# Performance work log

Measured on AMD Instinct MI355X. Metric: run time of the kernel, lower is better.

## Reference

```python
import jax, jax.numpy as jnp
import numpy as np

M, C, K, D = 2048, 16, 8, 256  # queries, classes, clusters/class, feature_dim
H1, H2 = D, D // 2             # MLP hidden sizes


def setup_inputs() -> dict:
    key = jax.random.key(0)
    ks = jax.random.split(key, 8)
    s1 = 1.0 / np.sqrt(2 * D)
    s2 = 1.0 / np.sqrt(H1)
    s3 = 1.0 / np.sqrt(H2)
    return {
        "query_features": jax.random.normal(ks[0], (M, D), jnp.float32),
        "prototypes": jax.random.normal(ks[1], (C, K, D), jnp.float32),
        "W1": jax.random.normal(ks[2], (2 * D, H1), jnp.float32) * s1,
        "b1": jnp.zeros((H1,), jnp.float32),
        "W2": jax.random.normal(ks[3], (H1, H2), jnp.float32) * s2,
        "b2": jnp.zeros((H2,), jnp.float32),
        "W3": jax.random.normal(ks[4], (H2, 1), jnp.float32) * s3,
        "b3": jnp.zeros((1,), jnp.float32),
    }


def reference(query_features, prototypes, W1, b1, W2, b2, W3, b3):
    # Attention MLP on concat([query, prototype]) for every (query, class, cluster)
    # pair. Split W1 into the query half and prototype half so we never
    # materialize the [M,C,K,2D] concat; broadcast-add instead.
    d = query_features.shape[-1]
    Wq, Wp = W1[:d], W1[d:]
    qh = query_features @ Wq                      # [M, H1]
    ph = jnp.einsum('ckd,dh->ckh', prototypes, Wp)  # [C, K, H1]
    h = jax.nn.relu(qh[:, None, None, :] + ph[None] + b1)   # [M, C, K, H1]
    h = jax.nn.relu(h @ W2 + b2)                              # [M, C, K, H2]
    scores = (h @ W3)[..., 0] + b3[0]                         # [M, C, K]
    attn = jax.nn.softmax(scores, axis=-1)                    # softmax over clusters
    weighted = jnp.einsum('mck,ckd->mcd', attn, prototypes)   # [M, C, D]
    diff = query_features[:, None, :] - weighted              # [M, C, D]
    distances = jnp.sqrt(jnp.sum(diff * diff, axis=-1))       # [M, C]
    return -distances
```

## Files before the change

kernel.cpp:

```cpp
#include <hip/hip_runtime.h>
#include <hip/hip_fp16.h>
#include <cstdint>

typedef __attribute__((ext_vector_type(8))) _Float16 f16x8;
typedef __attribute__((ext_vector_type(4))) float f32x4;
typedef __attribute__((ext_vector_type(16))) float f32x16;

__device__ __forceinline__ f16x8 cvt8(float4 x, float4 y) {
    f16x8 r;
    r[0] = (_Float16)x.x; r[1] = (_Float16)x.y; r[2] = (_Float16)x.z; r[3] = (_Float16)x.w;
    r[4] = (_Float16)y.x; r[5] = (_Float16)y.y; r[6] = (_Float16)y.z; r[7] = (_Float16)y.w;
    return r;
}

__device__ __forceinline__ f16x8 relu8(f16x8 v) {
    f16x8 z = {};
    return __builtin_elementwise_max(v, z);
}

__global__ __launch_bounds__(256)
void xpose(const float* __restrict__ query,
           const float* __restrict__ prot,
           const float* __restrict__ W1,
           const float* __restrict__ W2,
           const float* __restrict__ b2,
           _Float16* __restrict__ w1t,
           f16x8* __restrict__ w2p,
           float* __restrict__ Gm,
           float* __restrict__ q2) {
    int b = blockIdx.x, t = threadIdx.x;
    if (b < 32) {
        __shared__ _Float16 lt[64][73];
        int bi = b >> 2, bj = b & 3;
        int r0 = bi * 64, c0 = bj * 64;
        #pragma unroll
        for (int it = 0; it < 4; ++it) {
            int row = it * 16 + (t >> 4);
            int c4 = (t & 15) * 4;
            float4 v = *(const float4*)(W1 + (r0 + row) * 256 + c0 + c4);
            lt[row][c4]     = (_Float16)v.x;
            lt[row][c4 + 1] = (_Float16)v.y;
            lt[row][c4 + 2] = (_Float16)v.z;
            lt[row][c4 + 3] = (_Float16)v.w;
        }
        __syncthreads();
        int c = t >> 2, kq = t & 3;
        unsigned short o[16];
        #pragma unroll
        for (int i = 0; i < 16; ++i) {
            union { _Float16 f; unsigned short s; } u;
            u.f = lt[kq * 16 + i][c];
            o[i] = u.s;
        }
        _Float16* dst = w1t + (r0 >= 256 ? 65536 : 0) + (c0 + c) * 256 + (r0 & 255) + kq * 16;
        *(uint4*)dst       = *(uint4*)&o[0];
        *(uint4*)(dst + 8) = *(uint4*)&o[8];
    } else if (b < 49) {
        int chunk = (b - 32) * 256 + t;
        int ks = chunk >> 8, h = (chunk >> 7) & 1, c = chunk & 127;
        f16x8 o = {};
        if (ks < 16) {
            #pragma unroll
            for (int j = 0; j < 8; ++j)
                o[j] = (_Float16)W2[(ks * 16 + h * 8 + j) * 128 + c];
        } else if (h == 0) {
            o[0] = (_Float16)b2[c];
        }
        w2p[chunk] = o;
    } else if (b < 81) {
        int pid = (b - 49) * 32 + (t >> 3), l8 = t & 7;
        int c = pid >> 6, k = (pid >> 3) & 7, kp = pid & 7;
        const float4* pa = (const float4*)(prot + (c * 8 + k) * 256 + l8 * 32);
        const float4* pb = (const float4*)(prot + (c * 8 + kp) * 256 + l8 * 32);
        float s = 0.f;
        #pragma unroll
        for (int i = 0; i < 8; ++i) {
            float4 x = pa[i], y = pb[i];
            s += x.x * y.x + x.y * y.y + x.z * y.z + x.w * y.w;
        }
        s += __shfl_xor(s, 1); s += __shfl_xor(s, 2); s += __shfl_xor(s, 4);
        if (l8 == 0) Gm[pid] = s;
    } else {
        int m = (b - 81) * 32 + (t >> 3), l8 = t & 7;
        const float4* qp = (const float4*)(query + m * 256 + l8 * 32);
        float s = 0.f;
        #pragma unroll
        for (int i = 0; i < 8; ++i) {
            float4 x = qp[i];
            s += x.x * x.x + x.y * x.y + x.z * x.z + x.w * x.w;
        }
        s += __shfl_xor(s, 1); s += __shfl_xor(s, 2); s += __shfl_xor(s, 4);
        if (l8 == 0) q2[m] = s;
    }
}

__global__ __launch_bounds__(256, 2)
void prepg(const float* __restrict__ query,
           const float* __restrict__ prot,
           const _Float16* __restrict__ w1t,
           const float* __restrict__ b1,
           _Float16* __restrict__ qh16,
           float* __restrict__ sqp,
           _Float16* __restrict__ phpk) {
    int b = blockIdx.x, t = threadIdx.x;
    int w = t >> 6, l = t & 63, l15 = l & 15, l4 = l >> 4;
    int mode, row0, col0;
    if (b < 128)      { mode = 0; row0 = (b >> 2) * 64;         col0 = (b & 3) * 64; }
    else if (b < 192) { mode = 1; row0 = ((b - 128) >> 1) * 64; col0 = ((b - 128) & 1) * 64; }
    else              { mode = 2; row0 = ((b - 192) >> 2) * 64; col0 = ((b - 192) & 3) * 64; }
    const float* Asrc = (mode == 2) ? prot : query;
    const _Float16* Bsrc = (mode == 2) ? (w1t + 65536) : w1t;

    f32x4 acc[4];
    #pragma unroll
    for (int nt = 0; nt < 4; ++nt) acc[nt] = (f32x4){0.f, 0.f, 0.f, 0.f};

    for (int ks = 0; ks < 8; ++ks) {
        int row = row0 + w * 16 + l15;
        const float* ap = Asrc + row * 256 + ks * 32 + l4 * 8;
        f16x8 af = cvt8(*(const float4*)ap, *(const float4*)(ap + 4));
        f16x8 bf[4];
        #pragma unroll
        for (int nt = 0; nt < 4; ++nt) {
            int col = col0 + nt * 16 + l15;
            if (mode == 1) {
                const float* bp = prot + col * 256 + ks * 32 + l4 * 8;
                bf[nt] = cvt8(*(const float4*)bp, *(const float4*)(bp + 4));
            } else {
                bf[nt] = *(const f16x8*)(Bsrc + col * 256 + ks * 32 + l4 * 8);
            }
        }
        #pragma unroll
        for (int nt = 0; nt < 4; ++nt)
            acc[nt] = __builtin_amdgcn_mfma_f32_16x16x32_f16(af, bf[nt], acc[nt], 0, 0, 0);
    }
    #pragma unroll
    for (int nt = 0; nt < 4; ++nt)
        #pragma unroll
        for (int j = 0; j < 4; ++j) {
            int row = row0 + w * 16 + l4 * 4 + j;
            int col = col0 + nt * 16 + l15;
            float v = acc[nt][j];
            if (mode == 0)      qh16[row * 256 + col] = (_Float16)v;
            else if (mode == 1) sqp[row * 128 + col] = v;
            else                phpk[(((col >> 4) * 2 + ((col >> 3) & 1)) * 128 + row) * 8
                                     + (col & 7)] = (_Float16)(v + b1[col]);
        }
}

__global__ __launch_bounds__(1024, 1)
void fused3(const _Float16* __restrict__ qh16,
            const uint4* __restrict__ phpk,
            const uint4* __restrict__ w2p,
            const float* __restrict__ sqp,
            const float* __restrict__ q2,
            const float* __restrict__ Gm,
            const float* __restrict__ W3,
            float* __restrict__ out) {
    __shared__ uint4 w2l[4352];
    __shared__ uint4 phl[4096];
    __shared__ float w3l[128];
    __shared__ float spart[2][2][4][128];

    int t = threadIdx.x;
    int wid = t >> 6, l = t & 63;
    int rg = wid & 3, cs = wid >> 2;
    int lk = l & 31, h = l >> 5;
    int ck = rg * 32 + lk;

    for (int i = t; i < 4352; i += 1024) w2l[i] = w2p[i];
    for (int i = t; i < 4096; i += 1024) phl[i] = phpk[i];
    if (t < 128) w3l[t] = W3[t];
    __syncthreads();

    const _Float16* w2lh = (const _Float16*)w2l;
    const _Float16* phlh = (const _Float16*)phl;
    int m0 = blockIdx.x * 8;

    for (int mi = 0; mi < 4; ++mi) {
        int mA = m0 + mi * 2;
        const _Float16* qra = qh16 + mA * 256 + h * 8;
        const _Float16* qrb = qra + 256;

        f32x16 accA = {}, accB = {};

        f16x8 qa[2], qb[2];
        qa[0] = *(const f16x8*)(qra);
        qb[0] = *(const f16x8*)(qrb);
        qa[1] = *(const f16x8*)(qra + 16);
        qb[1] = *(const f16x8*)(qrb + 16);

        #pragma unroll
        for (int ks = 0; ks < 16; ++ks) {
            f16x8 ph = *(const f16x8*)(phlh + ((ks * 2 + h) * 128 + ck) * 8);
            f16x8 aA = relu8(qa[ks & 1] + ph);
            f16x8 aB = relu8(qb[ks & 1] + ph);
            if (ks < 14) {
                qa[ks & 1] = *(const f16x8*)(qra + (ks + 2) * 16);
                qb[ks & 1] = *(const f16x8*)(qrb + (ks + 2) * 16);
            }
            f16x8 bfr = *(const f16x8*)(w2lh + ((ks * 2 + h) * 128 + cs * 32 + lk) * 8);
            accA = __builtin_amdgcn_mfma_f32_32x32x16_f16(bfr, aA, accA, 0, 0, 0);
            accB = __builtin_amdgcn_mfma_f32_32x32x16_f16(bfr, aB, accB, 0, 0, 0);
        }
        {
            f16x8 e = {};
            if (h == 0) e[0] = (_Float16)1.0f;
            f16x8 bfr = *(const f16x8*)(w2lh + ((32 + h) * 128 + cs * 32 + lk) * 8);
            accA = __builtin_amdgcn_mfma_f32_32x32x16_f16(bfr, e, accA, 0, 0, 0);
            accB = __builtin_amdgcn_mfma_f32_32x32x16_f16(bfr, e, accB, 0, 0, 0);
        }

        int buf = mi & 1;
        {
            float s0 = 0.f, s1 = 0.f, s2 = 0.f, s3 = 0.f;
            #pragma unroll
            for (int r = 0; r < 16; r += 4) {
                s0 = fmaf(fmaxf(accA[r + 0], 0.f), w3l[cs * 32 + ((r + 0) & 3) + 8 * ((r + 0) >> 2) + 4 * h], s0);
                s1 = fmaf(fmaxf(accA[r + 1], 0.f), w3l[cs * 32 + ((r + 1) & 3) + 8 * ((r + 1) >> 2) + 4 * h], s1);
                s2 = fmaf(fmaxf(accA[r + 2], 0.f), w3l[cs * 32 + ((r + 2) & 3) + 8 * ((r + 2) >> 2) + 4 * h], s2);
                s3 = fmaf(fmaxf(accA[r + 3], 0.f), w3l[cs * 32 + ((r + 3) & 3) + 8 * ((r + 3) >> 2) + 4 * h], s3);
            }
            float s = (s0 + s1) + (s2 + s3);
            s += __shfl_xor(s, 32);
            if (l < 32) spart[buf][0][cs][ck] = s;
        }
        {
            float s0 = 0.f, s1 = 0.f, s2 = 0.f, s3 = 0.f;
            #pragma unroll
            for (int r = 0; r < 16; r += 4) {
                s0 = fmaf(fmaxf(accB[r + 0], 0.f), w3l[cs * 32 + ((r + 0) & 3) + 8 * ((r + 0) >> 2) + 4 * h], s0);
                s1 = fmaf(fmaxf(accB[r + 1], 0.f), w3l[cs * 32 + ((r + 1) & 3) + 8 * ((r + 1) >> 2) + 4 * h], s1);
                s2 = fmaf(fmaxf(accB[r + 2], 0.f), w3l[cs * 32 + ((r + 2) & 3) + 8 * ((r + 2) >> 2) + 4 * h], s2);
                s3 = fmaf(fmaxf(accB[r + 3], 0.f), w3l[cs * 32 + ((r + 3) & 3) + 8 * ((r + 3) >> 2) + 4 * h], s3);
            }
            float s = (s0 + s1) + (s2 + s3);
            s += __shfl_xor(s, 32);
            if (l < 32) spart[buf][1][cs][ck] = s;
        }
        __syncthreads();

        if (t < 256) {
            int msel = t >> 7, ckk = t & 127, kk = t & 7;
            int m = mA + msel;
            int cg = ckk >> 3;
            float s = spart[buf][msel][0][ckk] + spart[buf][msel][1][ckk]
                    + spart[buf][msel][2][ckk] + spart[buf][msel][3][ckk];
            float mx = s;
            mx = fmaxf(mx, __shfl_xor(mx, 1));
            mx = fmaxf(mx, __shfl_xor(mx, 2));
            mx = fmaxf(mx, __shfl_xor(mx, 4));
            float e = __expf(s - mx);
            float den = e;
            den += __shfl_xor(den, 1); den += __shfl_xor(den, 2); den += __shfl_xor(den, 4);
            float a = e / den;
            float p2 = a * sqp[m * 128 + ckk];
            float p3 = 0.f;
            #pragma unroll
            for (int kq = 0; kq < 8; ++kq) {
                float ak = __shfl(a, (l & 56) | kq);
                p3 = fmaf(ak, Gm[cg * 64 + kq * 8 + kk], p3);
            }
            p3 *= a;
            float pr = p3 - 2.f * p2;
            pr += __shfl_xor(pr, 1); pr += __shfl_xor(pr, 2); pr += __shfl_xor(pr, 4);
            if (kk == 0)
                out[m * 16 + cg] = -sqrtf(fmaxf(q2[m] + pr, 0.f));
        }
    }
}

extern "C" void kernel_launch(void* const* d_in, const int* in_sizes, int n_in,
                              void* d_out, int out_size, void* d_ws, size_t ws_size,
                              hipStream_t stream) {
    const float* query = (const float*)d_in[0];
    const float* prot  = (const float*)d_in[1];
    const float* W1    = (const float*)d_in[2];
    const float* b1    = (const float*)d_in[3];
    const float* W2    = (const float*)d_in[4];
    const float* b2    = (const float*)d_in[5];
    const float* W3    = (const float*)d_in[6];

    char* ws = (char*)d_ws;
    _Float16* qh16 = (_Float16*)(ws);
    _Float16* w1t  = (_Float16*)(ws + 1048576);
    f16x8*    w2p  = (f16x8*)(ws + 1310720);
    _Float16* phpk = (_Float16*)(ws + 1380352);
    float*    sqp  = (float*)(ws + 1445888);
    float*    q2   = (float*)(ws + 2494464);
    float*    Gm   = (float*)(ws + 2502656);
    float* out = (float*)d_out;

    xpose<<<145, 256, 0, stream>>>(query, prot, W1, W2, b2, w1t, w2p, Gm, q2);
    prepg<<<200, 256, 0, stream>>>(query, prot, w1t, b1, qh16, sqp, phpk);
    fused3<<<256, 1024, 0, stream>>>(qh16, (const uint4*)phpk, (const uint4*)w2p,
                                     sqp, q2, Gm, W3, out);
}
```

Baseline: 47.71 us.

## Split class-cluster dimension across blocks and keep W2/proto fragments in registers

```diff
diff --git a/kernel.cpp b/kernel.cpp
--- a/kernel.cpp
+++ b/kernel.cpp
@@ -148,8 +148,8 @@
         }
 }
 
-__global__ __launch_bounds__(1024, 1)
-void fused3(const _Float16* __restrict__ qh16,
+__global__ __launch_bounds__(512, 1)
+void fused4(const _Float16* __restrict__ qh16,
             const uint4* __restrict__ phpk,
             const uint4* __restrict__ w2p,
             const float* __restrict__ sqp,
@@ -157,58 +157,65 @@
             const float* __restrict__ Gm,
             const float* __restrict__ W3,
             float* __restrict__ out) {
-    __shared__ uint4 w2l[4352];
-    __shared__ uint4 phl[4096];
+    __shared__ _Float16 qlds[16 * 256];
     __shared__ float w3l[128];
-    __shared__ float spart[2][2][4][128];
+    __shared__ float spart[2][2][4][64];
 
     int t = threadIdx.x;
     int wid = t >> 6, l = t & 63;
-    int rg = wid & 3, cs = wid >> 2;
+    int rg = wid & 1, cs = wid >> 1;
     int lk = l & 31, h = l >> 5;
-    int ck = rg * 32 + lk;
-
-    for (int i = t; i < 4352; i += 1024) w2l[i] = w2p[i];
-    for (int i = t; i < 4096; i += 1024) phl[i] = phpk[i];
+    int ch = blockIdx.x & 1;
+    int mg = blockIdx.x >> 1;
+    int ckl = rg * 32 + lk;
+    int ck = ch * 64 + ckl;
+    int m0 = mg * 16;
+
+    const _Float16* w2h = (const _Float16*)w2p;
+    const _Float16* phh = (const _Float16*)phpk;
+
+    ((uint4*)qlds)[t] = ((const uint4*)(qh16 + m0 * 256))[t];
     if (t < 128) w3l[t] = W3[t];
+
+    f16x8 wA[17];
+    #pragma unroll
+    for (int ks = 0; ks < 17; ++ks)
+        wA[ks] = *(const f16x8*)(w2h + ((ks * 2 + h) * 128 + cs * 32 + lk) * 8);
+
+    f16x8 ph[16];
+    #pragma unroll
+    for (int ks = 0; ks < 16; ++ks)
+        ph[ks] = *(const f16x8*)(phh + ((ks * 2 + h) * 128 + ck) * 8);
+
     __syncthreads();
 
-    const _Float16* w2lh = (const _Float16*)w2l;
-    const _Float16* phlh = (const _Float16*)phl;
-    int m0 = blockIdx.x * 8;
-
-    for (int mi = 0; mi < 4; ++mi) {
+    for (int mi = 0; mi < 8; ++mi) {
         int mA = m0 + mi * 2;
-        const _Float16* qra = qh16 + mA * 256 + h * 8;
+        const _Float16* qra = qlds + (mi * 2) * 256 + h * 8;
         const _Float16* qrb = qra + 256;
 
         f32x16 accA = {}, accB = {};
 
         f16x8 qa[2], qb[2];
-        qa[0] = *(const f16x8*)(qra);
-        qb[0] = *(const f16x8*)(qrb);
-        qa[1] = *(const f16x8*)(qra + 16);
-        qb[1] = *(const f16x8*)(qrb + 16);
+        qa[0] = *(const f16x8*)(qra);       qb[0] = *(const f16x8*)(qrb);
+        qa[1] = *(const f16x8*)(qra + 16);  qb[1] = *(const f16x8*)(qrb + 16);
 
         #pragma unroll
         for (int ks = 0; ks < 16; ++ks) {
-            f16x8 ph = *(const f16x8*)(phlh + ((ks * 2 + h) * 128 + ck) * 8);
-            f16x8 aA = relu8(qa[ks & 1] + ph);
-            f16x8 aB = relu8(qb[ks & 1] + ph);
+            f16x8 aA = relu8(qa[ks & 1] + ph[ks]);
+            f16x8 aB = relu8(qb[ks & 1] + ph[ks]);
             if (ks < 14) {
                 qa[ks & 1] = *(const f16x8*)(qra + (ks + 2) * 16);
                 qb[ks & 1] = *(const f16x8*)(qrb + (ks + 2) * 16);
             }
-            f16x8 bfr = *(const f16x8*)(w2lh + ((ks * 2 + h) * 128 + cs * 32 + lk) * 8);
-            accA = __builtin_amdgcn_mfma_f32_32x32x16_f16(bfr, aA, accA, 0, 0, 0);
-            accB = __builtin_amdgcn_mfma_f32_32x32x16_f16(bfr, aB, accB, 0, 0, 0);
+            accA = __builtin_amdgcn_mfma_f32_32x32x16_f16(wA[ks], aA, accA, 0, 0, 0);
+            accB = __builtin_amdgcn_mfma_f32_32x32x16_f16(wA[ks], aB, accB, 0, 0, 0);
         }
         {
             f16x8 e = {};
             if (h == 0) e[0] = (_Float16)1.0f;
-            f16x8 bfr = *(const f16x8*)(w2lh + ((32 + h) * 128 + cs * 32 + lk) * 8);
-            accA = __builtin_amdgcn_mfma_f32_32x32x16_f16(bfr, e, accA, 0, 0, 0);
-            accB = __builtin_amdgcn_mfma_f32_32x32x16_f16(bfr, e, accB, 0, 0, 0);
+            accA = __builtin_amdgcn_mfma_f32_32x32x16_f16(wA[16], e, accA, 0, 0, 0);
+            accB = __builtin_amdgcn_mfma_f32_32x32x16_f16(wA[16], e, accB, 0, 0, 0);
         }
 
         int buf = mi & 1;
@@ -223,7 +230,7 @@
             }
             float s = (s0 + s1) + (s2 + s3);
             s += __shfl_xor(s, 32);
-            if (l < 32) spart[buf][0][cs][ck] = s;
+            if (l < 32) spart[buf][0][cs][ckl] = s;
         }
         {
             float s0 = 0.f, s1 = 0.f, s2 = 0.f, s3 = 0.f;
@@ -236,16 +243,16 @@
             }
             float s = (s0 + s1) + (s2 + s3);
             s += __shfl_xor(s, 32);
-            if (l < 32) spart[buf][1][cs][ck] = s;
+            if (l < 32) spart[buf][1][cs][ckl] = s;
         }
         __syncthreads();
 
-        if (t < 256) {
-            int msel = t >> 7, ckk = t & 127, kk = t & 7;
+        if (t < 128) {
+            int msel = t >> 6, cl = t & 63, kk = t & 7;
             int m = mA + msel;
-            int cg = ckk >> 3;
-            float s = spart[buf][msel][0][ckk] + spart[buf][msel][1][ckk]
-                    + spart[buf][msel][2][ckk] + spart[buf][msel][3][ckk];
+            int cg = ch * 8 + (cl >> 3);
+            float s = spart[buf][msel][0][cl] + spart[buf][msel][1][cl]
+                    + spart[buf][msel][2][cl] + spart[buf][msel][3][cl];
             float mx = s;
             mx = fmaxf(mx, __shfl_xor(mx, 1));
             mx = fmaxf(mx, __shfl_xor(mx, 2));
@@ -254,7 +261,7 @@
             float den = e;
             den += __shfl_xor(den, 1); den += __shfl_xor(den, 2); den += __shfl_xor(den, 4);
             float a = e / den;
-            float p2 = a * sqp[m * 128 + ckk];
+            float p2 = a * sqp[m * 128 + ch * 64 + cl];
             float p3 = 0.f;
             #pragma unroll
             for (int kq = 0; kq < 8; ++kq) {
@@ -293,6 +300,6 @@
 
     xpose<<<145, 256, 0, stream>>>(query, prot, W1, W2, b2, w1t, w2p, Gm, q2);
     prepg<<<200, 256, 0, stream>>>(query, prot, w1t, b1, qh16, sqp, phpk);
-    fused3<<<256, 1024, 0, stream>>>(qh16, (const uint4*)phpk, (const uint4*)w2p,
-                                     sqp, q2, Gm, W3, out);
-}
+    fused4<<<256, 512, 0, stream>>>(qh16, (const uint4*)phpk, (const uint4*)w2p,
+                                    sqp, q2, Gm, W3, out);
+}
```

Measured after the change: 42.78 us. -10.3%, faster.
